# Kernel tuning notes

Measured on AMD Instinct MI355X. Metric: run time of the kernel, lower is better.

The kernel has to match this reference:

```python
import jax, jax.numpy as jnp
import numpy as np

BOUND = 1.0
DENSITY_SCALE = 1.0
NUM_STEPS = 128
UPSAMPLE_STEPS = 128
MAX_FAR = 5.0
MIN_NEAR = 0.2


def setup_inputs() -> dict:
    key = jax.random.key(0)
    ks = jax.random.split(key, 10)
    N, H, G = 16384, 64, 15
    return {
        "rays_o": jax.random.normal(ks[0], (N, 3), jnp.float32) * 0.5,
        "rays_d": jax.random.normal(ks[1], (N, 3), jnp.float32),
        "W1": jax.random.normal(ks[2], (3, H), jnp.float32) * 0.5,
        "b1": jnp.zeros((H,), jnp.float32),
        "W2": jax.random.normal(ks[3], (H, 1 + G), jnp.float32) * 0.3,
        "b2": jnp.zeros((1 + G,), jnp.float32),
        "Wc1": jax.random.normal(ks[4], (3 + 3 + G, H), jnp.float32) * 0.3,
        "bc1": jnp.zeros((H,), jnp.float32),
        "Wc2": jax.random.normal(ks[5], (H, 3), jnp.float32) * 0.3,
        "bc2": jnp.zeros((3,), jnp.float32),
    }


def _density(x, W1, b1, W2, b2):
    # x: [P,3] -> sigma [P], geo_feat [P,G]
    h = jax.nn.relu(x @ W1 + b1)
    o = h @ W2 + b2
    return jax.nn.softplus(o[..., 0]), o[..., 1:]


def _color(x, d, geo, Wc1, bc1, Wc2, bc2):
    inp = jnp.concatenate([x, d, geo], axis=-1)
    h = jax.nn.relu(inp @ Wc1 + bc1)
    return jax.nn.sigmoid(h @ Wc2 + bc2)


def _near_far_from_aabb(o, d, lo, hi):
    ds = jnp.where(jnp.abs(d) < 1e-8, 1e-8, d)
    t1 = (lo - o) / ds
    t2 = (hi - o) / ds
    near = jnp.max(jnp.minimum(t1, t2), axis=-1)
    far = jnp.min(jnp.maximum(t1, t2), axis=-1)
    return near, far


def _composite(z_vals, sigma, sample_dist):
    # z_vals, sigma: [N,S]; sample_dist: [N,1]
    deltas = z_vals[..., 1:] - z_vals[..., :-1]
    deltas = jnp.concatenate([deltas, sample_dist * jnp.ones_like(deltas[..., :1])], axis=-1)
    alphas = 1.0 - jnp.exp(-deltas * DENSITY_SCALE * sigma)
    shifted = jnp.concatenate([jnp.ones_like(alphas[..., :1]), 1.0 - alphas + 1e-15], axis=-1)
    weights = alphas * jnp.cumprod(shifted, axis=-1)[..., :-1]
    return weights, deltas


def _sample_pdf(bins, weights, n_samples):
    # bins: [N,M+1], weights: [N,M]  (deterministic, det=True)
    weights = weights + 1e-5
    pdf = weights / jnp.sum(weights, axis=-1, keepdims=True)
    cdf = jnp.cumsum(pdf, axis=-1)
    cdf = jnp.concatenate([jnp.zeros_like(cdf[..., :1]), cdf], axis=-1)  # [N,M+1]
    M = cdf.shape[-1] - 1
    u = jnp.linspace(0.5 / n_samples, 1.0 - 0.5 / n_samples, n_samples, dtype=cdf.dtype)
    u = jnp.broadcast_to(u, cdf.shape[:-1] + (n_samples,))
    inds = jax.vmap(lambda c, uu: jnp.searchsorted(c, uu, side="right"))(cdf, u)
    below = jnp.maximum(inds - 1, 0)
    above = jnp.minimum(inds, M)
    cdf0 = jnp.take_along_axis(cdf, below, axis=-1)
    cdf1 = jnp.take_along_axis(cdf, above, axis=-1)
    b0 = jnp.take_along_axis(bins, below, axis=-1)
    b1 = jnp.take_along_axis(bins, above, axis=-1)
    denom = cdf1 - cdf0
    denom = jnp.where(denom < 1e-5, jnp.ones_like(denom), denom)
    t = (u - cdf0) / denom
    return b0 + t * (b1 - b0)


def reference(rays_o, rays_d, W1, b1, W2, b2, Wc1, bc1, Wc2, bc2):
    N = rays_o.shape[0]
    rays_d = rays_d / jnp.linalg.norm(rays_d, axis=-1, keepdims=True)
    lo = jnp.full((3,), -BOUND, rays_o.dtype)
    hi = jnp.full((3,), BOUND, rays_o.dtype)

    nears, fars = _near_far_from_aabb(rays_o, rays_d, lo, hi)
    fars = jnp.maximum(jnp.minimum(fars, MAX_FAR), MIN_NEAR)
    nears = jnp.minimum(jnp.maximum(nears, MIN_NEAR), MAX_FAR)
    nears = nears[:, None]
    fars = fars[:, None]

    z_vals = nears + (fars - nears) * jnp.linspace(0.0, 1.0, NUM_STEPS, dtype=rays_o.dtype)[None, :]
    sample_dist = (fars - nears) / NUM_STEPS  # [N,1]

    xyzs = rays_o[:, None, :] + rays_d[:, None, :] * z_vals[..., None]
    xyzs = jnp.clip(xyzs, lo, hi)
    sigma, geo = _density(xyzs.reshape(-1, 3), W1, b1, W2, b2)
    sigma = sigma.reshape(N, NUM_STEPS)
    geo = geo.reshape(N, NUM_STEPS, -1)

    # --- importance resampling (no_grad block in torch) ---
    w_c, deltas_c = _composite(z_vals, sigma, sample_dist)
    z_mid = z_vals[..., :-1] + 0.5 * deltas_c[..., :-1]
    new_z = _sample_pdf(z_mid, w_c[:, 1:-1], UPSAMPLE_STEPS)
    new_z = jax.lax.stop_gradient(new_z)
    new_xyzs = rays_o[:, None, :] + rays_d[:, None, :] * new_z[..., None]
    new_xyzs = jax.lax.stop_gradient(jnp.clip(new_xyzs, lo, hi))
    new_sigma, new_geo = _density(new_xyzs.reshape(-1, 3), W1, b1, W2, b2)
    new_sigma = new_sigma.reshape(N, UPSAMPLE_STEPS)
    new_geo = new_geo.reshape(N, UPSAMPLE_STEPS, -1)

    # merge + sort along sample axis
    z_all = jnp.concatenate([z_vals, new_z], axis=1)
    idx = jnp.argsort(z_all, axis=1)
    z_all = jnp.take_along_axis(z_all, idx, axis=1)
    xyz_all = jnp.take_along_axis(jnp.concatenate([xyzs, new_xyzs], axis=1), idx[..., None], axis=1)
    sigma_all = jnp.take_along_axis(jnp.concatenate([sigma, new_sigma], axis=1), idx, axis=1)
    geo_all = jnp.take_along_axis(jnp.concatenate([geo, new_geo], axis=1), idx[..., None], axis=1)

    weights, _ = _composite(z_all, sigma_all, sample_dist)
    S = z_all.shape[1]
    dirs = jnp.broadcast_to(rays_d[:, None, :], (N, S, 3))
    mask = weights > 1e-4
    rgb = _color(xyz_all.reshape(-1, 3), dirs.reshape(-1, 3), geo_all.reshape(-1, geo_all.shape[-1]), Wc1, bc1, Wc2, bc2)
    rgbs = jnp.where(mask.reshape(-1)[:, None], rgb, 0.0).reshape(N, S, 3)

    weights_sum = jnp.sum(weights, axis=-1)
    image = jnp.sum(weights[..., None] * rgbs, axis=-2)
    image = image + (1.0 - weights_sum)[..., None] * 1.0  # white bg
    return image
```

## Files before the change

kernel.cpp:

```cpp
#include <hip/hip_runtime.h>
#include <hip/hip_fp16.h>
#include <math.h>

#define NRAYS 16384
#define HID 64

typedef float    float4_ __attribute__((ext_vector_type(4)));
typedef _Float16 half8   __attribute__((ext_vector_type(8)));
typedef __fp16   fp16x2  __attribute__((ext_vector_type(2)));

__device__ __forceinline__ float clip1(float v){ return fminf(fmaxf(v,-1.f),1.f); }
__device__ __forceinline__ float softplusf_(float x){
  return fmaxf(x,0.f) + __logf(1.f + __expf(-fabsf(x)));
}
__device__ __forceinline__ float sigmoidf_(float x){
  return __fdividef(1.f, 1.f + __expf(-x));
}
__device__ __forceinline__ float h2f(unsigned short u){
  union { unsigned short s; __fp16 h; } cv; cv.s = u; return (float)cv.h;
}

__device__ __forceinline__ unsigned int pkh(float a, float b){
  union { fp16x2 h; unsigned int u; } cv;
  cv.h = __builtin_amdgcn_cvt_pkrtz(a, b);
  return cv.u;
}
__device__ __forceinline__ unsigned long long pk64(float4_ a){
  return (unsigned long long)pkh(a[0],a[1]) | ((unsigned long long)pkh(a[2],a[3])<<32);
}
__device__ __forceinline__ unsigned int relu_pk(unsigned int x){
  unsigned int y;
  __asm__("v_pk_max_f16 %0, %1, 0" : "=v"(y) : "v"(x));
  return y;
}

__device__ __forceinline__ void load_ray(const float* ro, const float* rd, int r,
    float& ox,float& oy,float& oz,float& dx,float& dy,float& dz){
  ox=ro[3*r]; oy=ro[3*r+1]; oz=ro[3*r+2];
  dx=rd[3*r]; dy=rd[3*r+1]; dz=rd[3*r+2];
  float inv = 1.f/sqrtf(dx*dx+dy*dy+dz*dz);
  dx*=inv; dy*=inv; dz*=inv;
}

__device__ __forceinline__ void aabb_nf(float ox,float oy,float oz,float dx,float dy,float dz,
    float& nears,float& fars){
  float dsx = (fabsf(dx)<1e-8f)?1e-8f:dx;
  float dsy = (fabsf(dy)<1e-8f)?1e-8f:dy;
  float dsz = (fabsf(dz)<1e-8f)?1e-8f:dz;
  float t1x=(-1.f-ox)/dsx, t2x=(1.f-ox)/dsx;
  float t1y=(-1.f-oy)/dsy, t2y=(1.f-oy)/dsy;
  float t1z=(-1.f-oz)/dsz, t2z=(1.f-oz)/dsz;
  float nr = fmaxf(fmaxf(fminf(t1x,t2x),fminf(t1y,t2y)),fminf(t1z,t2z));
  float fr = fminf(fminf(fmaxf(t1x,t2x),fmaxf(t1y,t2y)),fmaxf(t1z,t2z));
  fars  = fmaxf(fminf(fr,5.f),0.2f);
  nears = fminf(fmaxf(nr,0.2f),5.f);
}

__device__ __forceinline__ float wave_excl_chunk(float chunk, int lane, float& total){
  float incl = chunk;
  #pragma unroll
  for(int off=1; off<64; off<<=1){
    float n = __shfl_up(incl, off, 64);
    if (lane >= off) incl += n;
  }
  total = __shfl(incl, 63, 64);
  return incl - chunk;
}

__global__ void prep_weights(const float* __restrict__ W1, const float* __restrict__ W2,
                             const float* __restrict__ Wc1, const float* __restrict__ Wc2,
                             unsigned short* __restrict__ wb){
  int idx = blockIdx.x*256 + threadIdx.x;
  if (idx >= 6144) return;
  int f = idx>>3, j = idx&7, lane = f&63, slot = f>>6, q = lane>>4, c = lane&15;
  int k = q*8+j;
  float v = 0.f;
  if (slot < 4){        if (k<3) v = W1[k*HID + slot*16 + c]; }
  else if (slot < 6){   int h=(slot-4)*32+k; v = W2[h*16 + c]; }
  else if (slot < 10){  int mt=slot-6;
                        int row = (k==0)? -1 : (k<16 ? 5+k : (k<22 ? k-16 : -1));
                        if (row>=0) v = Wc1[row*HID + mt*16 + c]; }
  else {                int h=(slot-10)*32+k; if (c<3) v = Wc2[h*3 + c]; }
  wb[idx] = __half_as_ushort(__float2half_rn(v));
}

__device__ __forceinline__ void storeH(unsigned short* H, float4_ a, int t, int hbase){
  unsigned int lo = relu_pk(pkh(a[0],a[1]));
  unsigned int hi = relu_pk(pkh(a[2],a[3]));
  *(unsigned long long*)&H[hbase + t*256] =
      (unsigned long long)lo | ((unsigned long long)hi<<32);
}

__global__ __launch_bounds__(128) void nerf_fused(
    const float* __restrict__ ro, const float* __restrict__ rd,
    const float* __restrict__ b1, const float* __restrict__ b2,
    const float* __restrict__ bc1, const float* __restrict__ bc2,
    const unsigned short* __restrict__ wb, float* __restrict__ out)
{
  __shared__ __align__(16) unsigned short Hfrag[2][2][1024];
  __shared__ __align__(16) unsigned long long RGBS[2][256];
  __shared__ __align__(16) float zBs[2][128];
  __shared__ __align__(16) float zMc[2][260];

  const int tid = threadIdx.x, lane = tid&63, wv = tid>>6;
  const int q = lane>>4, c = lane&15;
  const int r = blockIdx.x*2 + wv;

  float ox,oy,oz,dx,dy,dz;
  load_ray(ro,rd,r,ox,oy,oz,dx,dy,dz);
  float nears,fars; aabb_nf(ox,oy,oz,dx,dy,dz,nears,fars);
  const float step  = (fars-nears)*(1.f/127.f);
  const float sdist = (fars-nears)*(1.f/128.f);
  const bool asc = (nears <= fars);
  const unsigned int pk_dydz = pkh(dy,dz);

  const half8* WF = (const half8*)wb;
  half8 aW1T[4], aW2T[2], aWc1T[4], aWc2T[2];
  #pragma unroll
  for(int t=0;t<4;t++){ aW1T[t] = WF[t*64+lane]; aWc1T[t] = WF[(6+t)*64+lane]; }
  #pragma unroll
  for(int k=0;k<2;k++){ aW2T[k] = WF[(4+k)*64+lane]; aWc2T[k] = WF[(10+k)*64+lane]; }
  float4_ b1v[4], bc1v[4];
  #pragma unroll
  for(int t=0;t<4;t++){
    b1v[t]  = *(const float4_*)&b1[t*16+q*4];
    bc1v[t] = *(const float4_*)&bc1[t*16+q*4];
  }
  const float4_ bTd = *(const float4_*)&b2[q*4];
  float4_ bTc = (float4_){0.f,0.f,0.f,0.f};
  if (q==0){ bTc[0]=bc2[0]; bTc[1]=bc2[1]; bTc[2]=bc2[2]; }

  unsigned short* H0 = &Hfrag[wv][0][0];
  unsigned short* H1 = &Hfrag[wv][1][0];
  unsigned long long* RGBSw = RGBS[wv];
  float* zBsw = zBs[wv];
  float* cdfw = zMc[wv];
  float* zMw  = zMc[wv];
  const int hbase  = (q>>1)*128 + c*8 + (q&1)*4;
  const int lread  = lane*8;
  const int gstage = c*16 + q*4;
  const int gread  = c*16 + q*8;

  auto pairbody = [&](int p, int sbase, bool coarse){
    const int sidx0 = p*32 + c, sidx1 = p*32 + 16 + c;
    half8 bf0 = (half8)(_Float16)0, bf1 = (half8)(_Float16)0;
    unsigned int c0a=0u,c0b=0u,c1a=0u,c1b=0u;
    if ((q&1)==0){
      float z0 = coarse ? fmaf(step,(float)sidx0,nears) : zBsw[sidx0];
      float z1 = coarse ? fmaf(step,(float)sidx1,nears) : zBsw[sidx1];
      float x0 = clip1(fmaf(dx,z0,ox)), y0 = clip1(fmaf(dy,z0,oy)), g0 = clip1(fmaf(dz,z0,oz));
      float x1 = clip1(fmaf(dx,z1,ox)), y1 = clip1(fmaf(dy,z1,oy)), g1 = clip1(fmaf(dz,z1,oz));
      if (q==0){
        unsigned int* u0p = (unsigned int*)&bf0;
        u0p[0] = pkh(x0,y0); u0p[1] = pkh(g0,0.f);
        unsigned int* u1p = (unsigned int*)&bf1;
        u1p[0] = pkh(x1,y1); u1p[1] = pkh(g1,0.f);
      } else {
        c0a = pkh(x0,y0); c0b = pkh(g0,dx);
        c1a = pkh(x1,y1); c1b = pkh(g1,dx);
      }
    }
    #pragma unroll
    for(int t=0;t<4;t++){
      float4_ a0 = __builtin_amdgcn_mfma_f32_16x16x32_f16(aW1T[t], bf0, b1v[t], 0,0,0);
      float4_ a1 = __builtin_amdgcn_mfma_f32_16x16x32_f16(aW1T[t], bf1, b1v[t], 0,0,0);
      storeH(H0, a0, t, hbase);
      storeH(H1, a1, t, hbase);
    }
    half8 h00 = *(const half8*)&H0[lread];
    half8 h01 = *(const half8*)&H0[512 + lread];
    half8 h10 = *(const half8*)&H1[lread];
    half8 h11 = *(const half8*)&H1[512 + lread];
    float4_ o0 = __builtin_amdgcn_mfma_f32_16x16x32_f16(aW2T[0], h00, bTd, 0,0,0);
    o0 = __builtin_amdgcn_mfma_f32_16x16x32_f16(aW2T[1], h01, o0, 0,0,0);
    float4_ o1 = __builtin_amdgcn_mfma_f32_16x16x32_f16(aW2T[0], h10, bTd, 0,0,0);
    o1 = __builtin_amdgcn_mfma_f32_16x16x32_f16(aW2T[1], h11, o1, 0,0,0);
    float sp0 = softplusf_(o0[0]);
    float sp1 = softplusf_(o1[0]);
    *(unsigned long long*)&H0[gstage] = pk64(o0);
    *(unsigned long long*)&H1[gstage] = pk64(o1);
    half8 bcf0 = (half8)(_Float16)0, bcf1 = (half8)(_Float16)0;
    if (q < 2){
      bcf0 = *(const half8*)&H0[gread];
      bcf1 = *(const half8*)&H1[gread];
    } else if (q == 2){
      unsigned int* u0p = (unsigned int*)&bcf0;
      u0p[0] = c0a; u0p[1] = c0b; u0p[2] = pk_dydz; u0p[3] = 0u;
      unsigned int* u1p = (unsigned int*)&bcf1;
      u1p[0] = c1a; u1p[1] = c1b; u1p[2] = pk_dydz; u1p[3] = 0u;
    }
    #pragma unroll
    for(int t=0;t<4;t++){
      float4_ a0 = __builtin_amdgcn_mfma_f32_16x16x32_f16(aWc1T[t], bcf0, bc1v[t], 0,0,0);
      float4_ a1 = __builtin_amdgcn_mfma_f32_16x16x32_f16(aWc1T[t], bcf1, bc1v[t], 0,0,0);
      storeH(H0, a0, t, hbase);
      storeH(H1, a1, t, hbase);
    }
    h00 = *(const half8*)&H0[lread];
    h01 = *(const half8*)&H0[512 + lread];
    h10 = *(const half8*)&H1[lread];
    h11 = *(const half8*)&H1[512 + lread];
    float4_ oc0 = __builtin_amdgcn_mfma_f32_16x16x32_f16(aWc2T[0], h00, bTc, 0,0,0);
    oc0 = __builtin_amdgcn_mfma_f32_16x16x32_f16(aWc2T[1], h01, oc0, 0,0,0);
    float4_ oc1 = __builtin_amdgcn_mfma_f32_16x16x32_f16(aWc2T[0], h10, bTc, 0,0,0);
    oc1 = __builtin_amdgcn_mfma_f32_16x16x32_f16(aWc2T[1], h11, oc1, 0,0,0);
    if (q==0){
      RGBSw[sbase+sidx0] = pk64((float4_){sigmoidf_(oc0[0]), sigmoidf_(oc0[1]),
                                          sigmoidf_(oc0[2]), sp0});
      RGBSw[sbase+sidx1] = pk64((float4_){sigmoidf_(oc1[0]), sigmoidf_(oc1[1]),
                                          sigmoidf_(oc1[2]), sp1});
    }
  };

  #pragma unroll
  for(int p=0;p<4;p++) pairbody(p, 0, true);

  {
    float s0 = h2f(((const unsigned short*)&RGBSw[2*lane  ])[3]);
    float s1 = h2f(((const unsigned short*)&RGBSw[2*lane+1])[3]);
    float d0 = (2*lane   < 127) ? step*s0 : 0.f;
    float d1 = (2*lane+1 < 127) ? step*s1 : 0.f;
    float tot;
    float e0 = wave_excl_chunk(d0+d1, lane, tot);
    float w0 = (1.f-__expf(-d0))*__expf(-e0);
    float w1 = (1.f-__expf(-d1))*__expf(-(e0+d0));
    float ww0 = (lane>=1 && 2*lane<127) ? w0+1e-5f : 0.f;
    float ww1 = (2*lane+1 < 127) ? w1+1e-5f : 0.f;
    float wsum;
    float ce0 = wave_excl_chunk(ww0+ww1, lane, wsum);
    float inv = __fdividef(1.f, wsum);
    cdfw[2*lane]   = (ce0+ww0)*inv;
    cdfw[2*lane+1] = (ce0+ww0+ww1)*inv;
  }

  {
    const float u0c = 0.5f/128.f;
    const float du = (1.f - 1.f/128.f)/127.f;
    #pragma unroll
    for(int j=0;j<2;j++){
      int k = lane + j*64;
      float u = fmaf(du,(float)k,u0c);
      int lo=0, hi=127;
      while(lo<hi){ int m=(lo+hi)>>1; if (cdfw[m] <= u) lo=m+1; else hi=m; }
      int below = max(lo-1,0), above = min(lo,126);
      float c0 = cdfw[below], c1 = cdfw[above];
      float bb0 = nears + step*((float)below + 0.5f);
      float bb1 = nears + step*((float)above + 0.5f);
      float den = c1 - c0; if (den < 1e-5f) den = 1.f;
      float zf = bb0 + (u - c0)/den*(bb1 - bb0);
      zBsw[asc ? k : 127-k] = zf;
    }
  }

  #pragma unroll
  for(int p=0;p<4;p++) pairbody(p, 128, false);

  #pragma unroll
  for(int j=0;j<2;j++){
    int sA = lane + j*64;
    int i = asc ? sA : 127-sA;
    float myz = fmaf(step,(float)i,nears);
    int lo=0, hi=128;
    while(lo<hi){ int m=(lo+hi)>>1; if (zBsw[m] < myz) lo=m+1; else hi=m; }
    int pos = sA + lo;
    zMw[pos] = __uint_as_float((__float_as_uint(myz) & ~255u) | (unsigned)i);
  }
  #pragma unroll
  for(int j=0;j<2;j++){
    int k = lane + j*64;
    float myz = zBsw[k];
    int lo=0, hi=128;
    while(lo<hi){
      int m=(lo+hi)>>1;
      float Am = fmaf(step,(float)(asc?m:127-m),nears);
      if (Am <= myz) lo=m+1; else hi=m;
    }
    int pos = k + lo;
    zMw[pos] = __uint_as_float((__float_as_uint(myz) & ~255u) | (unsigned)(128+k));
  }

  float accR=0.f, accG=0.f, accB=0.f, accW=0.f;
  {
    float4_ z4 = *(const float4_*)&zMw[4*lane];
    float z5 = zMw[4*lane+4];
    int oi0 = (int)(__float_as_uint(z4[0]) & 255u);
    int oi1 = (int)(__float_as_uint(z4[1]) & 255u);
    int oi2 = (int)(__float_as_uint(z4[2]) & 255u);
    int oi3 = (int)(__float_as_uint(z4[3]) & 255u);
    unsigned long long p0 = RGBSw[oi0];
    unsigned long long p1 = RGBSw[oi1];
    unsigned long long p2 = RGBSw[oi2];
    unsigned long long p3 = RGBSw[oi3];
    float sg0 = h2f((unsigned short)(p0>>48));
    float sg1 = h2f((unsigned short)(p1>>48));
    float sg2 = h2f((unsigned short)(p2>>48));
    float sg3 = h2f((unsigned short)(p3>>48));
    float d0 = (z4[1]-z4[0])*sg0;
    float d1 = (z4[2]-z4[1])*sg1;
    float d2 = (z4[3]-z4[2])*sg2;
    float dl = (lane==63) ? sdist : (z5 - z4[3]);
    float d3 = dl*sg3;
    float tot;
    float S = wave_excl_chunk(d0+d1+d2+d3, lane, tot);
    float4_ w4;
    w4[0] = (1.f-__expf(-d0))*__expf(-S); S += d0;
    w4[1] = (1.f-__expf(-d1))*__expf(-S); S += d1;
    w4[2] = (1.f-__expf(-d2))*__expf(-S); S += d2;
    w4[3] = (1.f-__expf(-d3))*__expf(-S);
    accW = w4[0]+w4[1]+w4[2]+w4[3];
    if (w4[0] > 1e-4f){
      accR = fmaf(w4[0], h2f((unsigned short) p0      ), accR);
      accG = fmaf(w4[0], h2f((unsigned short)(p0>>16) ), accG);
      accB = fmaf(w4[0], h2f((unsigned short)(p0>>32) ), accB);
    }
    if (w4[1] > 1e-4f){
      accR = fmaf(w4[1], h2f((unsigned short) p1      ), accR);
      accG = fmaf(w4[1], h2f((unsigned short)(p1>>16) ), accG);
      accB = fmaf(w4[1], h2f((unsigned short)(p1>>32) ), accB);
    }
    if (w4[2] > 1e-4f){
      accR = fmaf(w4[2], h2f((unsigned short) p2      ), accR);
      accG = fmaf(w4[2], h2f((unsigned short)(p2>>16) ), accG);
      accB = fmaf(w4[2], h2f((unsigned short)(p2>>32) ), accB);
    }
    if (w4[3] > 1e-4f){
      accR = fmaf(w4[3], h2f((unsigned short) p3      ), accR);
      accG = fmaf(w4[3], h2f((unsigned short)(p3>>16) ), accG);
      accB = fmaf(w4[3], h2f((unsigned short)(p3>>32) ), accB);
    }
  }

  #pragma unroll
  for(int off=32; off; off>>=1){
    accR += __shfl_down(accR, off, 64);
    accG += __shfl_down(accG, off, 64);
    accB += __shfl_down(accB, off, 64);
    accW += __shfl_down(accW, off, 64);
  }
  if (lane == 0){
    float bg = 1.f - accW;
    out[r*3+0] = accR + bg;
    out[r*3+1] = accG + bg;
    out[r*3+2] = accB + bg;
  }
}

extern "C" void kernel_launch(void* const* d_in, const int* in_sizes, int n_in,
                              void* d_out, int out_size, void* d_ws, size_t ws_size,
                              hipStream_t stream) {
  const float* ro  = (const float*)d_in[0];
  const float* rd  = (const float*)d_in[1];
  const float* W1  = (const float*)d_in[2];
  const float* b1  = (const float*)d_in[3];
  const float* W2  = (const float*)d_in[4];
  const float* b2  = (const float*)d_in[5];
  const float* Wc1 = (const float*)d_in[6];
  const float* bc1 = (const float*)d_in[7];
  const float* Wc2 = (const float*)d_in[8];
  const float* bc2 = (const float*)d_in[9];
  float* out = (float*)d_out;

  unsigned short* wb = (unsigned short*)d_ws;

  prep_weights<<<dim3(24), dim3(256), 0, stream>>>(W1, W2, Wc1, Wc2, wb);
  nerf_fused<<<dim3(NRAYS/2), dim3(128), 0, stream>>>(
      ro, rd, b1, b2, bc1, bc2, wb, out);
}
```

Before: 185.1 us.

## Cut LDS use, bpermute geo features, defer activations, direct-index merge search

Drops the separate zMc shared buffer by aliasing the cdf/merge scratch onto Hfrag, and adds a launch-bounds occupancy hint of 6. Geo features now reach the color-MLP B fragment through ds_bpermute instead of an LDS staging store and reload. Softplus and sigmoid are no longer applied in the MLP loop; raw fp16 outputs are stored and the activations run during compositing, where sigmoid is evaluated only for weights above threshold. The second merge binary search is replaced by a direct index from the uniform coarse spacing plus a small correction walk. Storing pre-activation values in fp16 changes rounding, and the tighter register bound may cause spills.

```diff
diff --git a/kernel.cpp b/kernel.cpp
--- a/kernel.cpp
+++ b/kernel.cpp
@@ -91,7 +91,7 @@
       (unsigned long long)lo | ((unsigned long long)hi<<32);
 }
 
-__global__ __launch_bounds__(128) void nerf_fused(
+__global__ __launch_bounds__(128, 6) void nerf_fused(
     const float* __restrict__ ro, const float* __restrict__ rd,
     const float* __restrict__ b1, const float* __restrict__ b2,
     const float* __restrict__ bc1, const float* __restrict__ bc2,
@@ -100,7 +100,6 @@
   __shared__ __align__(16) unsigned short Hfrag[2][2][1024];
   __shared__ __align__(16) unsigned long long RGBS[2][256];
   __shared__ __align__(16) float zBs[2][128];
-  __shared__ __align__(16) float zMc[2][260];
 
   const int tid = threadIdx.x, lane = tid&63, wv = tid>>6;
   const int q = lane>>4, c = lane&15;
@@ -134,12 +133,12 @@
   unsigned short* H1 = &Hfrag[wv][1][0];
   unsigned long long* RGBSw = RGBS[wv];
   float* zBsw = zBs[wv];
-  float* cdfw = zMc[wv];
-  float* zMw  = zMc[wv];
+  float* cdfw = (float*)&Hfrag[wv][0][0];
+  float* zMw  = (float*)&Hfrag[wv][0][0];
   const int hbase  = (q>>1)*128 + c*8 + (q&1)*4;
   const int lread  = lane*8;
-  const int gstage = c*16 + q*4;
-  const int gread  = c*16 + q*8;
+  const int ba0 = (q*32 + c)*4;
+  const int ba1 = ba0 + 64;
 
   auto pairbody = [&](int p, int sbase, bool coarse){
     const int sidx0 = p*32 + c, sidx1 = p*32 + 16 + c;
@@ -175,19 +174,24 @@
     o0 = __builtin_amdgcn_mfma_f32_16x16x32_f16(aW2T[1], h01, o0, 0,0,0);
     float4_ o1 = __builtin_amdgcn_mfma_f32_16x16x32_f16(aW2T[0], h10, bTd, 0,0,0);
     o1 = __builtin_amdgcn_mfma_f32_16x16x32_f16(aW2T[1], h11, o1, 0,0,0);
-    float sp0 = softplusf_(o0[0]);
-    float sp1 = softplusf_(o1[0]);
-    *(unsigned long long*)&H0[gstage] = pk64(o0);
-    *(unsigned long long*)&H1[gstage] = pk64(o1);
-    half8 bcf0 = (half8)(_Float16)0, bcf1 = (half8)(_Float16)0;
-    if (q < 2){
-      bcf0 = *(const half8*)&H0[gread];
-      bcf1 = *(const half8*)&H1[gread];
-    } else if (q == 2){
+    unsigned int pg0a = pkh(o0[0],o0[1]), pg0b = pkh(o0[2],o0[3]);
+    unsigned int pg1a = pkh(o1[0],o1[1]), pg1b = pkh(o1[2],o1[3]);
+    half8 bcf0, bcf1;
+    {
       unsigned int* u0p = (unsigned int*)&bcf0;
-      u0p[0] = c0a; u0p[1] = c0b; u0p[2] = pk_dydz; u0p[3] = 0u;
       unsigned int* u1p = (unsigned int*)&bcf1;
-      u1p[0] = c1a; u1p[1] = c1b; u1p[2] = pk_dydz; u1p[3] = 0u;
+      u0p[0] = (unsigned int)__builtin_amdgcn_ds_bpermute(ba0, (int)pg0a);
+      u0p[1] = (unsigned int)__builtin_amdgcn_ds_bpermute(ba0, (int)pg0b);
+      u0p[2] = (unsigned int)__builtin_amdgcn_ds_bpermute(ba1, (int)pg0a);
+      u0p[3] = (unsigned int)__builtin_amdgcn_ds_bpermute(ba1, (int)pg0b);
+      u1p[0] = (unsigned int)__builtin_amdgcn_ds_bpermute(ba0, (int)pg1a);
+      u1p[1] = (unsigned int)__builtin_amdgcn_ds_bpermute(ba0, (int)pg1b);
+      u1p[2] = (unsigned int)__builtin_amdgcn_ds_bpermute(ba1, (int)pg1a);
+      u1p[3] = (unsigned int)__builtin_amdgcn_ds_bpermute(ba1, (int)pg1b);
+      if (q == 2){
+        u0p[0] = c0a; u0p[1] = c0b; u0p[2] = pk_dydz; u0p[3] = 0u;
+        u1p[0] = c1a; u1p[1] = c1b; u1p[2] = pk_dydz; u1p[3] = 0u;
+      }
     }
     #pragma unroll
     for(int t=0;t<4;t++){
@@ -205,10 +209,8 @@
     float4_ oc1 = __builtin_amdgcn_mfma_f32_16x16x32_f16(aWc2T[0], h10, bTc, 0,0,0);
     oc1 = __builtin_amdgcn_mfma_f32_16x16x32_f16(aWc2T[1], h11, oc1, 0,0,0);
     if (q==0){
-      RGBSw[sbase+sidx0] = pk64((float4_){sigmoidf_(oc0[0]), sigmoidf_(oc0[1]),
-                                          sigmoidf_(oc0[2]), sp0});
-      RGBSw[sbase+sidx1] = pk64((float4_){sigmoidf_(oc1[0]), sigmoidf_(oc1[1]),
-                                          sigmoidf_(oc1[2]), sp1});
+      RGBSw[sbase+sidx0] = pk64((float4_){oc0[0], oc0[1], oc0[2], o0[0]});
+      RGBSw[sbase+sidx1] = pk64((float4_){oc1[0], oc1[1], oc1[2], o1[0]});
     }
   };
 
@@ -216,8 +218,10 @@
   for(int p=0;p<4;p++) pairbody(p, 0, true);
 
   {
-    float s0 = h2f(((const unsigned short*)&RGBSw[2*lane  ])[3]);
-    float s1 = h2f(((const unsigned short*)&RGBSw[2*lane+1])[3]);
+    unsigned long long e0u = RGBSw[2*lane];
+    unsigned long long e1u = RGBSw[2*lane+1];
+    float s0 = softplusf_(h2f((unsigned short)(e0u>>48)));
+    float s1 = softplusf_(h2f((unsigned short)(e1u>>48)));
     float d0 = (2*lane   < 127) ? step*s0 : 0.f;
     float d1 = (2*lane+1 < 127) ? step*s1 : 0.f;
     float tot;
@@ -265,16 +269,18 @@
     int pos = sA + lo;
     zMw[pos] = __uint_as_float((__float_as_uint(myz) & ~255u) | (unsigned)i);
   }
+  const float inv_step = (step != 0.f) ? __fdividef(1.f, step) : 0.f;
   #pragma unroll
   for(int j=0;j<2;j++){
     int k = lane + j*64;
     float myz = zBsw[k];
-    int lo=0, hi=128;
-    while(lo<hi){
-      int m=(lo+hi)>>1;
-      float Am = fmaf(step,(float)(asc?m:127-m),nears);
-      if (Am <= myz) lo=m+1; else hi=m;
-    }
+    float tt = (myz - nears)*inv_step;
+    float mr = (step == 0.f) ? 200.f : (asc ? tt : 127.f - tt);
+    mr = fminf(fmaxf(mr, -2.f), 130.f);
+    int lo = (int)floorf(mr) + 1;
+    lo = min(max(lo,0),128);
+    while (lo<128 && fmaf(step,(float)(asc?lo:127-lo),nears) <= myz) lo++;
+    while (lo>0  && fmaf(step,(float)(asc?(lo-1):(128-lo)),nears) >  myz) lo--;
     int pos = k + lo;
     zMw[pos] = __uint_as_float((__float_as_uint(myz) & ~255u) | (unsigned)(128+k));
   }
@@ -291,10 +297,10 @@
     unsigned long long p1 = RGBSw[oi1];
     unsigned long long p2 = RGBSw[oi2];
     unsigned long long p3 = RGBSw[oi3];
-    float sg0 = h2f((unsigned short)(p0>>48));
-    float sg1 = h2f((unsigned short)(p1>>48));
-    float sg2 = h2f((unsigned short)(p2>>48));
-    float sg3 = h2f((unsigned short)(p3>>48));
+    float sg0 = softplusf_(h2f((unsigned short)(p0>>48)));
+    float sg1 = softplusf_(h2f((unsigned short)(p1>>48)));
+    float sg2 = softplusf_(h2f((unsigned short)(p2>>48)));
+    float sg3 = softplusf_(h2f((unsigned short)(p3>>48)));
     float d0 = (z4[1]-z4[0])*sg0;
     float d1 = (z4[2]-z4[1])*sg1;
     float d2 = (z4[3]-z4[2])*sg2;
@@ -309,24 +315,24 @@
     w4[3] = (1.f-__expf(-d3))*__expf(-S);
     accW = w4[0]+w4[1]+w4[2]+w4[3];
     if (w4[0] > 1e-4f){
-      accR = fmaf(w4[0], h2f((unsigned short) p0      ), accR);
-      accG = fmaf(w4[0], h2f((unsigned short)(p0>>16) ), accG);
-      accB = fmaf(w4[0], h2f((unsigned short)(p0>>32) ), accB);
+      accR = fmaf(w4[0], sigmoidf_(h2f((unsigned short) p0      )), accR);
+      accG = fmaf(w4[0], sigmoidf_(h2f((unsigned short)(p0>>16))), accG);
+      accB = fmaf(w4[0], sigmoidf_(h2f((unsigned short)(p0>>32))), accB);
     }
     if (w4[1] > 1e-4f){
-      accR = fmaf(w4[1], h2f((unsigned short) p1      ), accR);
-      accG = fmaf(w4[1], h2f((unsigned short)(p1>>16) ), accG);
-      accB = fmaf(w4[1], h2f((unsigned short)(p1>>32) ), accB);
+      accR = fmaf(w4[1], sigmoidf_(h2f((unsigned short) p1      )), accR);
+      accG = fmaf(w4[1], sigmoidf_(h2f((unsigned short)(p1>>16))), accG);
+      accB = fmaf(w4[1], sigmoidf_(h2f((unsigned short)(p1>>32))), accB);
     }
     if (w4[2] > 1e-4f){
-      accR = fmaf(w4[2], h2f((unsigned short) p2      ), accR);
-      accG = fmaf(w4[2], h2f((unsigned short)(p2>>16) ), accG);
-      accB = fmaf(w4[2], h2f((unsigned short)(p2>>32) ), accB);
+      accR = fmaf(w4[2], sigmoidf_(h2f((unsigned short) p2      )), accR);
+      accG = fmaf(w4[2], sigmoidf_(h2f((unsigned short)(p2>>16))), accG);
+      accB = fmaf(w4[2], sigmoidf_(h2f((unsigned short)(p2>>32))), accB);
     }
     if (w4[3] > 1e-4f){
-      accR = fmaf(w4[3], h2f((unsigned short) p3      ), accR);
-      accG = fmaf(w4[3], h2f((unsigned short)(p3>>16) ), accG);
-      accB = fmaf(w4[3], h2f((unsigned short)(p3>>32) ), accB);
+      accR = fmaf(w4[3], sigmoidf_(h2f((unsigned short) p3      )), accR);
+      accG = fmaf(w4[3], sigmoidf_(h2f((unsigned short)(p3>>16))), accG);
+      accB = fmaf(w4[3], sigmoidf_(h2f((unsigned short)(p3>>32))), accB);
     }
   }
 
```

Result: slower. 559.8 us (+202.4%).
